# Performance work log

Hardware: AMD Instinct MI355X
Metric: run time of the kernel (lower is better)

The kernel has to match this reference:

```python
import jax, jax.numpy as jnp
import numpy as np

N = 4096          # num_nodes
E = 131072        # num_edges (avg degree 32)
H = 32            # hidden_channels
C_IN, C_OUT = 3, 3
DEPTH = 4
KS = [2000, 1000, 500, 250]  # ceil(ratio * n) per level, ratios = [2000/N, .5, .5, .5]


def gcn(x, A, W, b):
    """GCNConv with improved=True (self-loop fill 2, preserved if already present),
    symmetric normalization, aggregation out[dst] += norm * h[src]."""
    d = jnp.diagonal(A)
    A_hat = A + jnp.diag(jnp.where(d > 0, 0.0, 2.0))
    deg = A_hat.sum(0)                       # in-degree (col sums), as gcn_norm
    dis = jnp.where(deg > 0, jax.lax.rsqrt(deg), 0.0)
    msg = (x @ W) * dis[:, None]
    return (A_hat.T @ msg) * dis[:, None] + b


def augment(A):
    """GraphUNet.augment_adj: add self loops (w=1), square adjacency, drop self loops."""
    n = A.shape[0]
    eye = jnp.eye(n, dtype=A.dtype)
    A_sl = A + eye
    return (A_sl @ A_sl) * (1.0 - eye)


def pool(x, A, p, k):
    """TopKPooling: score = tanh((x.p)/||p||), keep top-k, gate x by score."""
    score = jnp.tanh((x @ p) / jnp.linalg.norm(p))
    vals, perm = jax.lax.top_k(score, k)
    return x[perm] * vals[:, None], A[perm][:, perm], perm


def setup_inputs() -> dict:
    key = jax.random.key(0)
    ks = jax.random.split(key, 12)
    x = jax.random.normal(ks[0], (N, C_IN), jnp.float32)
    edge_index = jax.random.randint(ks[1], (2, E), 0, N, dtype=jnp.int64)
    s = 0.1
    return {
        "x": x,
        "edge_index": edge_index,
        "W0": jax.random.normal(ks[2], (C_IN, H)) * s,
        "b0": jnp.zeros((H,), jnp.float32),
        "Wd": jax.random.normal(ks[3], (DEPTH, H, H)) * s,
        "bd": jnp.zeros((DEPTH, H), jnp.float32),
        "P": jax.random.normal(ks[4], (DEPTH, H)) * s,
        "Wu": jax.random.normal(ks[5], (DEPTH - 1, H, H)) * s,
        "bu": jnp.zeros((DEPTH - 1, H), jnp.float32),
        "Wlast": jax.random.normal(ks[6], (H, C_OUT)) * s,
        "blast": jnp.zeros((C_OUT,), jnp.float32),
    }


def reference(x, edge_index, W0, b0, Wd, bd, P, Wu, bu, Wlast, blast):
    # dense adjacency; duplicate edges accumulate like coalesced sparse weights
    A = jnp.zeros((N, N), jnp.float32).at[edge_index[0], edge_index[1]].add(1.0)
    x = jax.nn.relu(gcn(x, A, W0, b0))
    xs, As, perms = [x], [A], []
    for i in range(DEPTH):
        A = augment(A)
        x, A, perm = pool(x, A, P[i], KS[i])
        x = jax.nn.relu(gcn(x, A, Wd[i], bd[i]))
        if i < DEPTH - 1:
            xs.append(x)
            As.append(A)
        perms.append(perm)
    for i in range(DEPTH):
        j = DEPTH - 1 - i
        res = xs[j]
        up = jnp.zeros_like(res).at[perms[j]].set(x)  # unpool
        x = res + up                                   # sum_res=True
        if i < DEPTH - 1:
            x = jax.nn.relu(gcn(x, As[j], Wu[i], bu[i]))
        else:
            x = gcn(x, As[j], Wlast, blast)
    return jax.nn.log_softmax(x, axis=1)
```

## Files before the change

kernel.cpp:

```cpp
#include <hip/hip_runtime.h>
#include <math.h>

#define H 32
#define N0 4096
#define EMAX 131072
#define APSTR (4096 * 32)

typedef __attribute__((ext_vector_type(4))) float floatx4;
typedef __attribute__((ext_vector_type(8))) short short8;

__device__ __forceinline__ unsigned short f2bf_bits(float v) {
    union { float f; unsigned u; } c;
    c.f = v;
    unsigned lsb = (c.u >> 16) & 1u;
    c.u += 0x7fffu + lsb;
    return (unsigned short)(c.u >> 16);
}

__global__ void fill_sentinel_kernel(float* out, int n) {
    int t = blockIdx.x * 256 + threadIdx.x;
    if (t < n) out[t] = 9.0f;
}

__global__ void build_stats_kernel(const int* __restrict__ ei, int E, int* __restrict__ rowcnt,
                                   int* __restrict__ rowcntD, int* __restrict__ diagcnt) {
    int t = blockIdx.x * 256 + threadIdx.x;
    if (t >= E) return;
    int s = ei[t], d = ei[E + t];
    if ((unsigned)s >= N0 || (unsigned)d >= N0) return;
    atomicAdd(&rowcnt[s], 1);
    atomicAdd(&rowcntD[d], 1);
    if (s == d) atomicAdd(&diagcnt[s], 1);
}

__global__ __launch_bounds__(1024) void scan2_kernel(const int* __restrict__ cntA, int* __restrict__ rowpA,
                                                     int* __restrict__ curA, const int* __restrict__ cntB,
                                                     int* __restrict__ rowpB, int* __restrict__ curB) {
    __shared__ int part[1024];
    int tid = threadIdx.x;
    for (int pass = 0; pass < 2; pass++) {
        const int* cnt = pass ? cntB : cntA;
        int* rowp = pass ? rowpB : rowpA;
        int* cur = pass ? curB : curA;
        int base = tid * 4;
        int local[4];
        int s = 0;
#pragma unroll
        for (int i = 0; i < 4; i++) { local[i] = s; s += cnt[base + i]; }
        part[tid] = s;
        __syncthreads();
        for (int off = 1; off < 1024; off <<= 1) {
            int v = (tid >= off) ? part[tid - off] : 0;
            __syncthreads();
            part[tid] += v;
            __syncthreads();
        }
        int pre = (tid == 0) ? 0 : part[tid - 1];
#pragma unroll
        for (int i = 0; i < 4; i++) { rowp[base + i] = pre + local[i]; cur[base + i] = pre + local[i]; }
        if (tid == 1023) rowp[N0] = pre + s;
        __syncthreads();
    }
}

__global__ void fill_csr_kernel(const int* __restrict__ ei, int E, int* __restrict__ cursor,
                                int* __restrict__ cols, int* __restrict__ cursorD,
                                int* __restrict__ srcs) {
    int t = blockIdx.x * 256 + threadIdx.x;
    if (t >= E) return;
    int s = ei[t], d = ei[E + t];
    if ((unsigned)s >= N0 || (unsigned)d >= N0) return;
    int pos = atomicAdd(&cursor[s], 1);
    cols[pos] = d;
    int posD = atomicAdd(&cursorD[d], 1);
    srcs[posD] = s;
}

__global__ __launch_bounds__(256) void aug0_kernel(const int* __restrict__ rowp, const int* __restrict__ cols,
                                                   const int* __restrict__ perm, const int* __restrict__ invperm,
                                                   int kOut, int ldC, float* __restrict__ C) {
    __shared__ float row[2048];
    int a = blockIdx.x;
    int tid = threadIdx.x;
    for (int j = tid; j < ldC; j += 256) row[j] = 0.f;
    __syncthreads();
    if (a < kOut) {
        int pa = perm[a];
        int s0 = rowp[pa], s1 = rowp[pa + 1];
        for (int e = s0 + tid; e < s1; e += 256) {
            int k = cols[e];
            int ip = invperm[k];
            if (ip >= 0) atomicAdd(&row[ip], 2.0f);
            int t1 = rowp[k + 1];
            for (int e2 = rowp[k]; e2 < t1; ++e2) {
                int ip2 = invperm[cols[e2]];
                if (ip2 >= 0) atomicAdd(&row[ip2], 1.0f);
            }
        }
    }
    __syncthreads();
    for (int j = tid; j < ldC; j += 256) C[(long)a * ldC + j] = (j == a) ? 0.f : row[j];
}

__global__ void gather_rows_kernel(const float* __restrict__ M, int ldM, const int* __restrict__ perm,
                                   int kOut, float* __restrict__ Gr) {
    int k = blockIdx.x * 256 + threadIdx.x;
    int a = blockIdx.y;
    if (k >= ldM) return;
    float v = 0.f;
    if (a < kOut) {
        int pa = perm[a];
        v = M[(long)pa * ldM + k] + (k == pa ? 1.f : 0.f);
    }
    Gr[(long)a * ldM + k] = v;
}

__global__ void gather_rows_bf16_kernel(const float* __restrict__ M, int ldM, const int* __restrict__ perm,
                                        int kOut, unsigned short* __restrict__ Gr) {
    int k = blockIdx.x * 256 + threadIdx.x;
    int a = blockIdx.y;
    if (k >= ldM) return;
    float v = 0.f;
    if (a < kOut) {
        int pa = perm[a];
        v = M[(long)pa * ldM + k] + (k == pa ? 1.f : 0.f);
    }
    Gr[(long)a * ldM + k] = f2bf_bits(v);
}

__global__ void gather_cols_kernel(const float* __restrict__ M, int ldM, const int* __restrict__ perm,
                                   int kOut, float* __restrict__ Gc, int ldC) {
    int b = blockIdx.x * 256 + threadIdx.x;
    int k = blockIdx.y;
    if (b >= ldC) return;
    float v = 0.f;
    if (b < kOut) {
        int pb = perm[b];
        v = M[(long)k * ldM + pb] + (k == pb ? 1.f : 0.f);
    }
    Gc[(long)k * ldC + b] = v;
}

__global__ void gather_colsT_bf16_kernel(const float* __restrict__ M, int ldM,
                                         const int* __restrict__ perm, int kOut,
                                         unsigned short* __restrict__ GcT) {
    __shared__ float t[32][33];
    __shared__ int pb[32];
    int b0 = blockIdx.x * 32, k0 = blockIdx.y * 32;
    int tx = threadIdx.x, ty = threadIdx.y;
    if (ty == 0) pb[tx] = (b0 + tx < kOut) ? perm[b0 + tx] : -1;
    __syncthreads();
    for (int y = ty; y < 32; y += 8) {
        int k = k0 + y;
        int pbx = pb[tx];
        float v = 0.f;
        if (pbx >= 0) v = M[(long)k * ldM + pbx] + (k == pbx ? 1.f : 0.f);
        t[y][tx] = v;
    }
    __syncthreads();
    for (int y = ty; y < 32; y += 8)
        GcT[(long)(b0 + y) * ldM + k0 + tx] = f2bf_bits(t[tx][y]);
}

__global__ __launch_bounds__(256) void mfma_aug_kernel(const unsigned short* __restrict__ Aop,
                                                       const unsigned short* __restrict__ Bop,
                                                       float* __restrict__ C, int K, int ldC, int kchunk) {
    __shared__ __align__(16) unsigned short lA[64 * 32];
    __shared__ __align__(16) unsigned short lB[64 * 32];
    const int tid = threadIdx.x;
    const int lane = tid & 63;
    const int w = tid >> 6;
    const int a0 = blockIdx.y * 64, b0 = blockIdx.x * 64;
    const int kbase = blockIdx.z * kchunk;
    const int r0 = tid >> 2;
    const int c8 = (tid & 3) * 8;
    const unsigned short* gA = Aop + (long)(a0 + r0) * K + kbase + c8;
    const unsigned short* gB = Bop + (long)(b0 + r0) * K + kbase + c8;
    const int wm = (w & 1) * 32;
    const int wn = (w >> 1) * 32;
    const int lm = lane & 15;
    const int quad = lane >> 4;
    floatx4 acc[2][2];
#pragma unroll
    for (int i = 0; i < 2; i++)
#pragma unroll
        for (int j = 0; j < 2; j++) {
            floatx4 z = {0.f, 0.f, 0.f, 0.f};
            acc[i][j] = z;
        }
    for (int k0 = 0; k0 < kchunk; k0 += 32) {
        short8 va = *(const short8*)(gA + k0);
        short8 vb = *(const short8*)(gB + k0);
        __syncthreads();
        *(short8*)&lA[r0 * 32 + c8] = va;
        *(short8*)&lB[r0 * 32 + c8] = vb;
        __syncthreads();
        short8 af[2], bf[2];
#pragma unroll
        for (int mi = 0; mi < 2; mi++) af[mi] = *(const short8*)&lA[(wm + mi * 16 + lm) * 32 + quad * 8];
#pragma unroll
        for (int ni = 0; ni < 2; ni++) bf[ni] = *(const short8*)&lB[(wn + ni * 16 + lm) * 32 + quad * 8];
#pragma unroll
        for (int mi = 0; mi < 2; mi++)
#pragma unroll
            for (int ni = 0; ni < 2; ni++)
                acc[mi][ni] = __builtin_amdgcn_mfma_f32_16x16x32_bf16(af[mi], bf[ni], acc[mi][ni], 0, 0, 0);
    }
#pragma unroll
    for (int mi = 0; mi < 2; mi++)
#pragma unroll
        for (int ni = 0; ni < 2; ni++) {
            int col = b0 + wn + ni * 16 + lm;
#pragma unroll
            for (int r = 0; r < 4; r++) {
                int row = a0 + wm + mi * 16 + quad * 4 + r;
                if (row != col) atomicAdd(&C[(long)row * ldC + col], acc[mi][ni][r]);
            }
        }
}

__global__ __launch_bounds__(256) void gemm64_kernel(const float* __restrict__ Gr,
                                                     const float* __restrict__ Gc,
                                                     float* __restrict__ Cpart, int K, int ldC, int kchunk) {
    __shared__ float As[32][68];
    __shared__ float Bs[32][68];
    const int tid = threadIdx.x;
    const int a0 = blockIdx.y * 64, b0 = blockIdx.x * 64;
    const int kbase = blockIdx.z * kchunk;
    float* Cz = Cpart + (long)blockIdx.z * ldC * ldC;
    const int tx = tid & 15, ty = tid >> 4;
    const int lr = tid >> 2;
    const int lk = (tid & 3) * 8;
    const int bb = tid & 63;
    const int kr = (tid >> 6) * 8;
    const float* gA = Gr + (long)(a0 + lr) * K + lk + kbase;
    const float* gB = Gc + (long)(kr + kbase) * ldC + b0 + bb;
    float acc[4][4];
#pragma unroll
    for (int i = 0; i < 4; i++)
#pragma unroll
        for (int j = 0; j < 4; j++) acc[i][j] = 0.f;
    for (int k0 = 0; k0 < kchunk; k0 += 32) {
        float a8[8], b8[8];
#pragma unroll
        for (int i = 0; i < 8; i++) a8[i] = gA[k0 + i];
#pragma unroll
        for (int i = 0; i < 8; i++) b8[i] = gB[(long)(k0 + i) * ldC];
        __syncthreads();
#pragma unroll
        for (int i = 0; i < 8; i++) As[lk + i][lr] = a8[i];
#pragma unroll
        for (int i = 0; i < 8; i++) Bs[kr + i][bb] = b8[i];
        __syncthreads();
#pragma unroll
        for (int k = 0; k < 32; k++) {
            floatx4 av = *(const floatx4*)&As[k][ty * 4];
            floatx4 bv = *(const floatx4*)&Bs[k][tx * 4];
#pragma unroll
            for (int i = 0; i < 4; i++)
#pragma unroll
                for (int j = 0; j < 4; j++) acc[i][j] += av[i] * bv[j];
        }
    }
#pragma unroll
    for (int i = 0; i < 4; i++)
#pragma unroll
        for (int j = 0; j < 4; j++) {
            int a = a0 + ty * 4 + i, b = b0 + tx * 4 + j;
            Cz[(long)a * ldC + b] = acc[i][j];
        }
}

__global__ void reduce_part_kernel(const float* __restrict__ Cpart, float* __restrict__ C,
                                   int ldC, int ksplit) {
    int t = blockIdx.x * 256 + threadIdx.x;
    long tot = (long)ldC * ldC;
    if (t >= tot) return;
    float s = 0.f;
    for (int z = 0; z < ksplit; z++) s += Cpart[(long)z * tot + t];
    int a = t / ldC, b = t % ldC;
    C[t] = (a == b) ? 0.f : s;
}

__global__ void colsum_part_kernel(const float* __restrict__ A, float* __restrict__ degp, int ld) {
    int i = blockIdx.x * 256 + threadIdx.x;
    int jb = blockIdx.y;
    int j0 = jb * 64;
    float s0 = 0.f, s1 = 0.f, s2 = 0.f, s3 = 0.f, s4 = 0.f, s5 = 0.f, s6 = 0.f, s7 = 0.f;
    const float* p = A + (long)j0 * ld + i;
#pragma unroll
    for (int jq = 0; jq < 64; jq += 8) {
        float v[8];
#pragma unroll
        for (int q = 0; q < 8; q++) v[q] = p[(long)(jq + q) * ld];
        s0 += v[0]; s1 += v[1]; s2 += v[2]; s3 += v[3];
        s4 += v[4]; s5 += v[5]; s6 += v[6]; s7 += v[7];
    }
    float s = ((s0 + s1) + (s2 + s3)) + ((s4 + s5) + (s6 + s7));
    degp[(long)jb * ld + i] = s;
}

__global__ void msgg_kernel(const float* __restrict__ x, const int* __restrict__ perm,
                            const float* __restrict__ vals, const float* __restrict__ xup,
                            const int* __restrict__ invp, const float* __restrict__ Wb,
                            const float* __restrict__ A, int ld, const float* __restrict__ degp,
                            int nparts, float* __restrict__ dis, float* __restrict__ fixb,
                            float* __restrict__ msg, int n) {
    int idx = blockIdx.x * 256 + threadIdx.x;
    if (idx >= n * 32) return;
    int i = idx >> 5, c = idx & 31;
    float di, fx;
    if (degp) {
        float dsum = 0.f;
        for (int z = 0; z < nparts; z++) dsum += degp[(long)z * ld + i];
        float diag = A[(long)i * ld + i];
        fx = diag > 0.f ? 0.f : 2.f;
        float dg = dsum + fx;
        di = dg > 0.f ? 1.f / sqrtf(dg) : 0.f;
        if (c == 0) { dis[i] = di; fixb[i] = fx; }
    } else {
        di = dis[i];
        fx = fixb[i];
    }
    int src = perm ? perm[i] : i;
    float vs = vals ? vals[i] : 1.f;
    int ip = invp ? invp[i] : -1;
    float s = 0.f;
#pragma unroll
    for (int q = 0; q < 32; q++) {
        float xv = x[(long)src * 32 + q];
        if (ip >= 0) xv += xup[(long)ip * 32 + q];
        s += xv * Wb[q * 32 + c];
    }
    msg[idx] = s * vs * di;
    (void)fx;
}

__global__ __launch_bounds__(256) void aggT_kernel(const float* __restrict__ A,
                                                   const float* __restrict__ msg,
                                                   float* __restrict__ aggp, int n, int ld, int jchunk) {
    __shared__ float As[64][64];
    __shared__ float Ms[64][32];
    const int tid = threadIdx.x;
    const int i0 = blockIdx.x * 64;
    const int il = tid & 63;
    const int cg = tid >> 6;
    const int i = i0 + il;
    const int mrow = tid >> 2;
    const int mc = (tid & 3) * 8;
    float acc[8];
#pragma unroll
    for (int q = 0; q < 8; q++) acc[q] = 0.f;
    const int j0 = blockIdx.y * jchunk;
    for (int jb = j0; jb < j0 + jchunk; jb += 64) {
        float a16[16], m8[8];
#pragma unroll
        for (int q = 0; q < 16; q++) a16[q] = A[(long)(jb + cg + 4 * q) * ld + i0 + il];
#pragma unroll
        for (int q = 0; q < 8; q++) m8[q] = msg[(long)(jb + mrow) * 32 + mc + q];
        __syncthreads();
#pragma unroll
        for (int q = 0; q < 16; q++) As[cg + 4 * q][il] = a16[q];
#pragma unroll
        for (int q = 0; q < 8; q++) Ms[mrow][mc + q] = m8[q];
        __syncthreads();
#pragma unroll
        for (int jl = 0; jl < 64; jl++) {
            float a = As[jl][il];
#pragma unroll
            for (int q = 0; q < 8; q++) acc[q] += a * Ms[jl][cg * 8 + q];
        }
        __syncthreads();
    }
    if (i < n) {
#pragma unroll
        for (int q = 0; q < 8; q++) aggp[(long)blockIdx.y * APSTR + (long)i * 32 + cg * 8 + q] = acc[q];
    }
}

__global__ void epi_sum_kernel(const float* __restrict__ aggp, int jsplit, const float* __restrict__ msg,
                               const float* __restrict__ dis, const float* __restrict__ fixb,
                               const float* __restrict__ bb, float* __restrict__ out, int n, int relu,
                               const float* __restrict__ p, int npow,
                               unsigned long long* __restrict__ keys) {
    __shared__ float psh[32];
    if (p) {
        if (threadIdx.x < 32) psh[threadIdx.x] = p[threadIdx.x];
        __syncthreads();
    }
    int idx = blockIdx.x * 256 + threadIdx.x;
    int tot = (p ? npow : n) * 32;
    if (idx >= tot) return;
    int i = idx >> 5, c = idx & 31;
    float v = 0.f;
    if (i < n) {
        float s = 0.f;
        for (int z = 0; z < jsplit; z++) s += aggp[(long)z * APSTR + idx];
        v = (s + fixb[i] * msg[idx]) * dis[i] + bb[c];
        if (relu) v = fmaxf(v, 0.f);
        out[idx] = v;
    }
    if (p) {
        float pc = psh[c];
        float d = v * pc;
        float nq = pc * pc;
#pragma unroll
        for (int st = 16; st >= 1; st >>= 1) {
            d += __shfl_xor(d, st);
            nq += __shfl_xor(nq, st);
        }
        if (c == 0) {
            unsigned long long kk = 0ULL;
            if (i < n) {
                float sc = tanhf(d / sqrtf(nq));
                unsigned u = __float_as_uint(sc);
                u = (u & 0x80000000u) ? ~u : (u | 0x80000000u);
                kk = ((unsigned long long)u << 32) | (unsigned)(~i);
            }
            keys[i] = kk;
        }
    }
}

__global__ void msg0_kernel(const float* __restrict__ x, const float* __restrict__ Wb,
                            const int* __restrict__ rowcntD, const int* __restrict__ diagcnt,
                            float* __restrict__ dis, float* __restrict__ fixb,
                            float* __restrict__ msg, int n) {
    int idx = blockIdx.x * 256 + threadIdx.x;
    if (idx >= n * 32) return;
    int i = idx >> 5, c = idx & 31;
    float fx = diagcnt[i] > 0 ? 0.f : 2.f;
    float dg = (float)rowcntD[i] + fx;
    float di = dg > 0.f ? 1.f / sqrtf(dg) : 0.f;
    if (c == 0) { dis[i] = di; fixb[i] = fx; }
    float s = x[i * 3] * Wb[c] + x[i * 3 + 1] * Wb[32 + c] + x[i * 3 + 2] * Wb[64 + c];
    msg[idx] = s * di;
}

__global__ void msg3up_kernel(const float* __restrict__ res, const float* __restrict__ xup,
                              const int* __restrict__ invp, const float* __restrict__ Wb,
                              const float* __restrict__ dis, float* __restrict__ msg, int n) {
    int idx = blockIdx.x * 256 + threadIdx.x;
    if (idx >= n * 3) return;
    int i = idx / 3, c = idx % 3;
    int ip = invp[i];
    float s = 0.f;
#pragma unroll
    for (int q = 0; q < 32; q++) {
        float xv = res[(long)i * 32 + q];
        if (ip >= 0) xv += xup[(long)ip * 32 + q];
        s += xv * Wb[q * 3 + c];
    }
    msg[idx] = s * dis[i];
}

__global__ void cscagg_epi_keys_kernel(const int* __restrict__ rowpD, const int* __restrict__ srcs,
                                       const float* __restrict__ msg, const float* __restrict__ dis,
                                       const float* __restrict__ fixb, const float* __restrict__ bb,
                                       float* __restrict__ out, int n, const float* __restrict__ p,
                                       unsigned long long* __restrict__ keys) {
    __shared__ float psh[32];
    if (threadIdx.x < 32) psh[threadIdx.x] = p[threadIdx.x];
    __syncthreads();
    int idx = blockIdx.x * 256 + threadIdx.x;
    if (idx >= n * 32) return;
    int i = idx >> 5, c = idx & 31;
    float acc = 0.f;
    int e0 = rowpD[i], e1 = rowpD[i + 1];
    for (int e = e0; e < e1; e++) acc += msg[(long)srcs[e] * 32 + c];
    float v = (acc + fixb[i] * msg[idx]) * dis[i] + bb[c];
    v = fmaxf(v, 0.f);
    out[idx] = v;
    float pc = psh[c];
    float d = v * pc;
    float nq = pc * pc;
#pragma unroll
    for (int st = 16; st >= 1; st >>= 1) {
        d += __shfl_xor(d, st);
        nq += __shfl_xor(nq, st);
    }
    if (c == 0) {
        float sc = tanhf(d / sqrtf(nq));
        unsigned u = __float_as_uint(sc);
        u = (u & 0x80000000u) ? ~u : (u | 0x80000000u);
        keys[i] = ((unsigned long long)u << 32) | (unsigned)(~i);
    }
}

__global__ void cscagg_lsm_kernel(const int* __restrict__ rowpD, const int* __restrict__ srcs,
                                  const float* __restrict__ msg, const float* __restrict__ dis,
                                  const float* __restrict__ fixb, const float* __restrict__ bb,
                                  float* __restrict__ out, int n) {
    int i = blockIdx.x * 256 + threadIdx.x;
    if (i >= n) return;
    float a0 = 0.f, a1 = 0.f, a2 = 0.f;
    int e0 = rowpD[i], e1 = rowpD[i + 1];
    for (int e = e0; e < e1; e++) {
        const float* m = &msg[(long)srcs[e] * 3];
        a0 += m[0]; a1 += m[1]; a2 += m[2];
    }
    float di = dis[i], fx = fixb[i];
    float v0 = (a0 + fx * msg[i * 3]) * di + bb[0];
    float v1 = (a1 + fx * msg[i * 3 + 1]) * di + bb[1];
    float v2 = (a2 + fx * msg[i * 3 + 2]) * di + bb[2];
    float m = fmaxf(v0, fmaxf(v1, v2));
    float s = expf(v0 - m) + expf(v1 - m) + expf(v2 - m);
    float l = m + logf(s);
    out[i * 3] = v0 - l;
    out[i * 3 + 1] = v1 - l;
    out[i * 3 + 2] = v2 - l;
}

__global__ __launch_bounds__(256) void topk_rank_kernel(const unsigned long long* __restrict__ keys,
                                                        int npow, int k, int* __restrict__ perm,
                                                        float* __restrict__ vals,
                                                        int* __restrict__ invperm) {
    __shared__ unsigned long long ks[4096];
    __shared__ int psum[256];
    const int tid = threadIdx.x;
    for (int t = tid; t < npow; t += 256) ks[t] = keys[t];
    __syncthreads();
    const int m = tid & 15;
    const int chunk = tid >> 4;
    const int myi = blockIdx.x * 16 + m;
    unsigned long long my = ks[myi];
    const int cl = npow >> 4;
    const unsigned long long* base = &ks[chunk * cl];
    int r = 0;
#pragma unroll 4
    for (int j = 0; j < cl; j++) r += (base[j] > my) ? 1 : 0;
    psum[chunk * 16 + m] = r;
    __syncthreads();
    if (tid < 16) {
        int mk_i = blockIdx.x * 16 + tid;
        unsigned long long mk = ks[mk_i];
        int rank = 0;
#pragma unroll
        for (int c = 0; c < 16; c++) rank += psum[c * 16 + tid];
        invperm[mk_i] = (rank < k) ? rank : -1;
        if (rank < k) {
            perm[rank] = (int)(~(unsigned)mk);
            unsigned u = (unsigned)(mk >> 32);
            u = (u & 0x80000000u) ? (u ^ 0x80000000u) : ~u;
            vals[rank] = __uint_as_float(u);
        }
    }
}

static void run_gcn_dense(hipStream_t st, const float* A, int n, int ld, const float* x,
                          const int* perm, const float* vals, const float* xup, const int* invp,
                          const float* Wt, const float* bt, int relu, float* out, float* degp,
                          float* aggp, float* dis, float* fixb, float* msgb, int computeDeg,
                          const float* pnext, int npow_next, unsigned long long* keys) {
    if (computeDeg) {
        dim3 gcs(ld / 256 > 0 ? ld / 256 : 1, ld / 64);
        colsum_part_kernel<<<gcs, 256, 0, st>>>(A, degp, ld);
    }
    int gm = (n * H + 255) / 256;
    msgg_kernel<<<gm, 256, 0, st>>>(x, perm, vals, xup, invp, Wt, A, ld,
                                    computeDeg ? degp : nullptr, ld / 64, dis, fixb, msgb, n);
    int jsplit = ld / 256 > 0 ? ld / 256 : 1;
    int ajc = ld / jsplit;
    dim3 ga(ld / 64, jsplit);
    aggT_kernel<<<ga, 256, 0, st>>>(A, msgb, aggp, n, ld, ajc);
    int gme = ((pnext ? npow_next : n) * H + 255) / 256;
    epi_sum_kernel<<<gme, 256, 0, st>>>(aggp, jsplit, msgb, dis, fixb, bt, out, n, relu,
                                        pnext, npow_next, keys);
}

extern "C" void kernel_launch(void* const* d_in, const int* in_sizes, int n_in,
                              void* d_out, int out_size, void* d_ws, size_t ws_size,
                              hipStream_t stream) {
    const float* x0f = (const float*)d_in[0];
    const int* eidx = (const int*)d_in[1];
    const float* W0f = (const float*)d_in[2];
    const float* b0f = (const float*)d_in[3];
    const float* Wdf = (const float*)d_in[4];
    const float* bdf = (const float*)d_in[5];
    const float* Pf = (const float*)d_in[6];
    const float* Wuf = (const float*)d_in[7];
    const float* buf2 = (const float*)d_in[8];
    const float* Wlf = (const float*)d_in[9];
    const float* blf = (const float*)d_in[10];
    const int E = in_sizes[1] / 2;

    unsigned char* w = (unsigned char*)d_ws;
    size_t off = 0;
    auto alloc = [&](size_t bytes) -> void* {
        void* p = w + off;
        off += (bytes + 255) & ~(size_t)255;
        return p;
    };
    int* rowcnt = (int*)alloc(N0 * 4);
    int* rowcntD = (int*)alloc(N0 * 4);
    int* diagcnt = (int*)alloc(N0 * 4);
    int* rowp = (int*)alloc((N0 + 1) * 4);
    int* rowpD = (int*)alloc((N0 + 1) * 4);
    int* cursor = (int*)alloc(N0 * 4);
    int* cursorD = (int*)alloc(N0 * 4);
    int* cols = (int*)alloc((size_t)EMAX * 4);
    int* srcs = (int*)alloc((size_t)EMAX * 4);
    float* dis0 = (float*)alloc(N0 * 4);
    float* fixb0 = (float*)alloc(N0 * 4);
    unsigned long long* keys = (unsigned long long*)alloc((size_t)N0 * 8);
    float* A1 = (float*)alloc((size_t)2048 * 2048 * 4);
    float* A2 = (float*)alloc((size_t)1024 * 1024 * 4);
    float* A3 = (float*)alloc((size_t)512 * 512 * 4);
    float* A4 = (float*)alloc((size_t)256 * 256 * 4);
    float* Gr = (float*)alloc((size_t)1024 * 2048 * 4);
    float* Gc = (float*)alloc((size_t)2048 * 1024 * 4);
    unsigned short* Grb = (unsigned short*)alloc((size_t)1024 * 2048 * 2);
    unsigned short* GcTb = (unsigned short*)alloc((size_t)1024 * 2048 * 2);
    float* Cpart = (float*)alloc((size_t)8 * 512 * 512 * 4);
    float* degp = (float*)alloc((size_t)32 * 2048 * 4);
    float* aggp = (float*)alloc((size_t)8 * APSTR * 4);
    float* xs0 = (float*)alloc((size_t)N0 * H * 4);
    float* xs1 = (float*)alloc((size_t)2000 * H * 4);
    float* xs2 = (float*)alloc((size_t)1000 * H * 4);
    float* xs3 = (float*)alloc((size_t)500 * H * 4);
    float* xtB = (float*)alloc((size_t)N0 * H * 4);
    float* xtC = (float*)alloc((size_t)N0 * H * 4);
    float* msgb = (float*)alloc((size_t)N0 * H * 4);
    float* disL = (float*)alloc((size_t)4 * N0 * 4);
    float* fixbL = (float*)alloc((size_t)4 * N0 * 4);
    int* invpermL = (int*)alloc((size_t)4 * N0 * 4);
    const int ksz[4] = {2000, 1000, 500, 250};
    int* perm[4];
    float* vals[4];
    for (int i = 0; i < 4; i++) perm[i] = (int*)alloc((size_t)ksz[i] * 4);
    for (int i = 0; i < 4; i++) vals[i] = (float*)alloc((size_t)ksz[i] * 4);

    if (off > ws_size) {
        fill_sentinel_kernel<<<(out_size + 255) / 256, 256, 0, stream>>>((float*)d_out, out_size);
        return;
    }

    const int nlvl[5] = {N0, 2000, 1000, 500, 250};
    const int ldl[5] = {N0, 2048, 1024, 512, 256};
    const int npw[4] = {4096, 2048, 1024, 512};
    float* Afp[5] = {nullptr, A1, A2, A3, A4};
    float* xsb[4] = {xs0, xs1, xs2, xs3};

    hipMemsetAsync(rowcnt, 0, (size_t)N0 * 3 * 4, stream);
    build_stats_kernel<<<(E + 255) / 256, 256, 0, stream>>>(eidx, E, rowcnt, rowcntD, diagcnt);
    scan2_kernel<<<1, 1024, 0, stream>>>(rowcnt, rowp, cursor, rowcntD, rowpD, cursorD);
    fill_csr_kernel<<<(E + 255) / 256, 256, 0, stream>>>(eidx, E, cursor, cols, cursorD, srcs);

    msg0_kernel<<<(N0 * H + 255) / 256, 256, 0, stream>>>(x0f, W0f, rowcntD, diagcnt, dis0, fixb0,
                                                          msgb, N0);
    cscagg_epi_keys_kernel<<<(N0 * H + 255) / 256, 256, 0, stream>>>(rowpD, srcs, msgb, dis0, fixb0,
                                                                     b0f, xs0, N0, Pf, keys);
    float* xcur = xs0;

    for (int i = 0; i < 4; ++i) {
        int kk = ksz[i], ldn = ldl[i + 1];
        topk_rank_kernel<<<npw[i] / 16, 256, 0, stream>>>(keys, npw[i], kk, perm[i], vals[i],
                                                          invpermL + i * N0);
        if (i == 0) {
            aug0_kernel<<<ldn, 256, 0, stream>>>(rowp, cols, perm[0], invpermL, kk, ldn, A1);
        } else if (i == 1) {
            int ldM = ldl[i];
            dim3 gr((ldM + 255) / 256, ldn);
            gather_rows_bf16_kernel<<<gr, 256, 0, stream>>>(Afp[i], ldM, perm[i], kk, Grb);
            dim3 gt(ldn / 32, ldM / 32);
            gather_colsT_bf16_kernel<<<gt, dim3(32, 8), 0, stream>>>(Afp[i], ldM, perm[i], kk, GcTb);
            hipMemsetAsync(Afp[i + 1], 0, (size_t)ldn * ldn * 4, stream);
            int ksplit = 4;
            int kchunk = ldM / ksplit;
            dim3 gg(ldn / 64, ldn / 64, ksplit);
            mfma_aug_kernel<<<gg, 256, 0, stream>>>(Grb, GcTb, Afp[i + 1], ldM, ldn, kchunk);
        } else {
            int ldM = ldl[i];
            dim3 gr((ldM + 255) / 256, ldn);
            gather_rows_kernel<<<gr, 256, 0, stream>>>(Afp[i], ldM, perm[i], kk, Gr);
            dim3 gc((ldn + 255) / 256, ldM);
            gather_cols_kernel<<<gc, 256, 0, stream>>>(Afp[i], ldM, perm[i], kk, Gc, ldn);
            int ksplit = 8;
            int kchunk = ldM / ksplit;
            dim3 gg(ldn / 64, ldn / 64, ksplit);
            gemm64_kernel<<<gg, 256, 0, stream>>>(Gr, Gc, Cpart, ldM, ldn, kchunk);
            long tot = (long)ldn * ldn;
            reduce_part_kernel<<<(tot + 255) / 256, 256, 0, stream>>>(Cpart, Afp[i + 1], ldn, ksplit);
        }
        float* outx = (i < 3) ? xsb[i + 1] : xtB;
        const float* pnext = (i < 3) ? (Pf + (i + 1) * H) : nullptr;
        int npow_next = (i < 3) ? npw[i + 1] : 0;
        run_gcn_dense(stream, Afp[i + 1], kk, ldn, xcur, perm[i], vals[i], nullptr, nullptr,
                      Wdf + i * (H * H), bdf + i * H, 1, outx, degp, aggp, disL + i * N0,
                      fixbL + i * N0, msgb, 1, pnext, npow_next, keys);
        xcur = outx;
    }

    for (int i = 0; i < 4; ++i) {
        int j = 3 - i;
        int nj = nlvl[j];
        if (i < 3) {
            float* outx = (xcur == xtB) ? xtC : xtB;
            run_gcn_dense(stream, Afp[j], nj, ldl[j], xsb[j], nullptr, nullptr, xcur,
                          invpermL + j * N0, Wuf + i * (H * H), buf2 + i * H, 1, outx, degp, aggp,
                          disL + (j - 1) * N0, fixbL + (j - 1) * N0, msgb, 0, nullptr, 0, nullptr);
            xcur = outx;
        } else {
            msg3up_kernel<<<(N0 * 3 + 255) / 256, 256, 0, stream>>>(xs0, xcur, invpermL, Wlf, dis0,
                                                                    msgb, N0);
            cscagg_lsm_kernel<<<(N0 + 255) / 256, 256, 0, stream>>>(rowpD, srcs, msgb, dis0, fixb0,
                                                                    blf, (float*)d_out, N0);
        }
    }
}
```

Baseline: 443.0 us.

## Fuse per-level GCN stages into one persistent kernel with grid barriers

```diff
diff --git a/kernel.cpp b/kernel.cpp
--- a/kernel.cpp
+++ b/kernel.cpp
@@ -15,6 +15,24 @@
     unsigned lsb = (c.u >> 16) & 1u;
     c.u += 0x7fffu + lsb;
     return (unsigned short)(c.u >> 16);
+}
+
+__device__ __forceinline__ void grid_bar(int* bar) {
+    __threadfence();
+    __syncthreads();
+    if (threadIdx.x == 0) {
+        int g = __hip_atomic_load(&bar[1], __ATOMIC_RELAXED, __HIP_MEMORY_SCOPE_AGENT);
+        int t = __hip_atomic_fetch_add(&bar[0], 1, __ATOMIC_ACQ_REL, __HIP_MEMORY_SCOPE_AGENT);
+        if (t == (int)gridDim.x - 1) {
+            __hip_atomic_store(&bar[0], 0, __ATOMIC_RELAXED, __HIP_MEMORY_SCOPE_AGENT);
+            __hip_atomic_store(&bar[1], g + 1, __ATOMIC_RELEASE, __HIP_MEMORY_SCOPE_AGENT);
+        } else {
+            while (__hip_atomic_load(&bar[1], __ATOMIC_ACQUIRE, __HIP_MEMORY_SCOPE_AGENT) == g)
+                __builtin_amdgcn_s_sleep(1);
+        }
+    }
+    __syncthreads();
+    __threadfence();
 }
 
 __global__ void fill_sentinel_kernel(float* out, int n) {
@@ -63,17 +81,34 @@
     }
 }
 
-__global__ void fill_csr_kernel(const int* __restrict__ ei, int E, int* __restrict__ cursor,
-                                int* __restrict__ cols, int* __restrict__ cursorD,
-                                int* __restrict__ srcs) {
-    int t = blockIdx.x * 256 + threadIdx.x;
-    if (t >= E) return;
-    int s = ei[t], d = ei[E + t];
-    if ((unsigned)s >= N0 || (unsigned)d >= N0) return;
-    int pos = atomicAdd(&cursor[s], 1);
-    cols[pos] = d;
-    int posD = atomicAdd(&cursorD[d], 1);
-    srcs[posD] = s;
+__global__ void fillcsr_msg0_kernel(const int* __restrict__ ei, int E, int* __restrict__ cursor,
+                                    int* __restrict__ cols, int* __restrict__ cursorD,
+                                    int* __restrict__ srcs, const float* __restrict__ x,
+                                    const float* __restrict__ Wb, const int* __restrict__ rcntD,
+                                    const int* __restrict__ diagcnt, float* __restrict__ dis,
+                                    float* __restrict__ fixb, float* __restrict__ msg, int n) {
+    int nf = (E + 255) >> 8;
+    int tid = threadIdx.x;
+    if ((int)blockIdx.x < nf) {
+        int t = blockIdx.x * 256 + tid;
+        if (t >= E) return;
+        int s = ei[t], d = ei[E + t];
+        if ((unsigned)s >= N0 || (unsigned)d >= N0) return;
+        int pos = atomicAdd(&cursor[s], 1);
+        cols[pos] = d;
+        int posD = atomicAdd(&cursorD[d], 1);
+        srcs[posD] = s;
+    } else {
+        int idx = ((int)blockIdx.x - nf) * 256 + tid;
+        if (idx >= n * 32) return;
+        int i = idx >> 5, c = idx & 31;
+        float fx = diagcnt[i] > 0 ? 0.f : 2.f;
+        float dg = (float)rcntD[i] + fx;
+        float di = dg > 0.f ? 1.f / sqrtf(dg) : 0.f;
+        if (c == 0) { dis[i] = di; fixb[i] = fx; }
+        float s = x[i * 3] * Wb[c] + x[i * 3 + 1] * Wb[32 + c] + x[i * 3 + 2] * Wb[64 + c];
+        msg[idx] = s * di;
+    }
 }
 
 __global__ __launch_bounds__(256) void aug0_kernel(const int* __restrict__ rowp, const int* __restrict__ cols,
@@ -102,64 +137,72 @@
     for (int j = tid; j < ldC; j += 256) C[(long)a * ldC + j] = (j == a) ? 0.f : row[j];
 }
 
-__global__ void gather_rows_kernel(const float* __restrict__ M, int ldM, const int* __restrict__ perm,
-                                   int kOut, float* __restrict__ Gr) {
-    int k = blockIdx.x * 256 + threadIdx.x;
-    int a = blockIdx.y;
-    if (k >= ldM) return;
-    float v = 0.f;
-    if (a < kOut) {
-        int pa = perm[a];
-        v = M[(long)pa * ldM + k] + (k == pa ? 1.f : 0.f);
-    }
-    Gr[(long)a * ldM + k] = v;
-}
-
-__global__ void gather_rows_bf16_kernel(const float* __restrict__ M, int ldM, const int* __restrict__ perm,
-                                        int kOut, unsigned short* __restrict__ Gr) {
-    int k = blockIdx.x * 256 + threadIdx.x;
-    int a = blockIdx.y;
-    if (k >= ldM) return;
-    float v = 0.f;
-    if (a < kOut) {
-        int pa = perm[a];
-        v = M[(long)pa * ldM + k] + (k == pa ? 1.f : 0.f);
-    }
-    Gr[(long)a * ldM + k] = f2bf_bits(v);
-}
-
-__global__ void gather_cols_kernel(const float* __restrict__ M, int ldM, const int* __restrict__ perm,
-                                   int kOut, float* __restrict__ Gc, int ldC) {
-    int b = blockIdx.x * 256 + threadIdx.x;
-    int k = blockIdx.y;
-    if (b >= ldC) return;
-    float v = 0.f;
-    if (b < kOut) {
-        int pb = perm[b];
-        v = M[(long)k * ldM + pb] + (k == pb ? 1.f : 0.f);
-    }
-    Gc[(long)k * ldC + b] = v;
-}
-
-__global__ void gather_colsT_bf16_kernel(const float* __restrict__ M, int ldM,
-                                         const int* __restrict__ perm, int kOut,
-                                         unsigned short* __restrict__ GcT) {
+__global__ void gatherAB_bf16_kernel(const float* __restrict__ M, int ldM, const int* __restrict__ perm,
+                                     int kOut, unsigned short* __restrict__ Gr,
+                                     unsigned short* __restrict__ GcT, int ldn) {
     __shared__ float t[32][33];
     __shared__ int pb[32];
-    int b0 = blockIdx.x * 32, k0 = blockIdx.y * 32;
-    int tx = threadIdx.x, ty = threadIdx.y;
-    if (ty == 0) pb[tx] = (b0 + tx < kOut) ? perm[b0 + tx] : -1;
-    __syncthreads();
-    for (int y = ty; y < 32; y += 8) {
-        int k = k0 + y;
-        int pbx = pb[tx];
+    int half = (ldM >> 8) * ldn;
+    int u = blockIdx.x;
+    int tid = threadIdx.x;
+    if (u < half) {
+        int gx = ldM >> 8;
+        int a = u / gx;
+        int k = (u % gx) * 256 + tid;
         float v = 0.f;
-        if (pbx >= 0) v = M[(long)k * ldM + pbx] + (k == pbx ? 1.f : 0.f);
-        t[y][tx] = v;
-    }
-    __syncthreads();
-    for (int y = ty; y < 32; y += 8)
-        GcT[(long)(b0 + y) * ldM + k0 + tx] = f2bf_bits(t[tx][y]);
+        if (a < kOut) {
+            int pa = perm[a];
+            v = M[(long)pa * ldM + k] + (k == pa ? 1.f : 0.f);
+        }
+        Gr[(long)a * ldM + k] = f2bf_bits(v);
+    } else {
+        u -= half;
+        int nbx = ldn >> 5;
+        int bx = u % nbx, by = u / nbx;
+        int b0 = bx * 32, k0 = by * 32;
+        int tx = tid & 31, ty = tid >> 5;
+        if (ty == 0) pb[tx] = (b0 + tx < kOut) ? perm[b0 + tx] : -1;
+        __syncthreads();
+        for (int y = ty; y < 32; y += 8) {
+            int k = k0 + y;
+            int pbx = pb[tx];
+            float v = 0.f;
+            if (pbx >= 0) v = M[(long)k * ldM + pbx] + (k == pbx ? 1.f : 0.f);
+            t[y][tx] = v;
+        }
+        __syncthreads();
+        for (int y = ty; y < 32; y += 8)
+            GcT[(long)(b0 + y) * ldM + k0 + tx] = f2bf_bits(t[tx][y]);
+    }
+}
+
+__global__ void gather_both_kernel(const float* __restrict__ M, int ldM, const int* __restrict__ perm,
+                                   int kOut, float* __restrict__ Gr, float* __restrict__ Gc, int ldn) {
+    int half = (ldM >> 8) * ldn;
+    int u = blockIdx.x;
+    int tid = threadIdx.x;
+    if (u < half) {
+        int gx = ldM >> 8;
+        int a = u / gx;
+        int k = (u % gx) * 256 + tid;
+        float v = 0.f;
+        if (a < kOut) {
+            int pa = perm[a];
+            v = M[(long)pa * ldM + k] + (k == pa ? 1.f : 0.f);
+        }
+        Gr[(long)a * ldM + k] = v;
+    } else {
+        u -= half;
+        int gx = ldn >> 8;
+        int k = u / gx;
+        int b = (u % gx) * 256 + tid;
+        float v = 0.f;
+        if (b < kOut) {
+            int pb2 = perm[b];
+            v = M[(long)k * ldM + pb2] + (k == pb2 ? 1.f : 0.f);
+        }
+        Gc[(long)k * ldn + b] = v;
+    }
 }
 
 __global__ __launch_bounds__(256) void mfma_aug_kernel(const unsigned short* __restrict__ Aop,
@@ -282,176 +325,200 @@
     C[t] = (a == b) ? 0.f : s;
 }
 
-__global__ void colsum_part_kernel(const float* __restrict__ A, float* __restrict__ degp, int ld) {
-    int i = blockIdx.x * 256 + threadIdx.x;
-    int jb = blockIdx.y;
-    int j0 = jb * 64;
-    float s0 = 0.f, s1 = 0.f, s2 = 0.f, s3 = 0.f, s4 = 0.f, s5 = 0.f, s6 = 0.f, s7 = 0.f;
-    const float* p = A + (long)j0 * ld + i;
-#pragma unroll
-    for (int jq = 0; jq < 64; jq += 8) {
-        float v[8];
-#pragma unroll
-        for (int q = 0; q < 8; q++) v[q] = p[(long)(jq + q) * ld];
-        s0 += v[0]; s1 += v[1]; s2 += v[2]; s3 += v[3];
-        s4 += v[4]; s5 += v[5]; s6 += v[6]; s7 += v[7];
-    }
-    float s = ((s0 + s1) + (s2 + s3)) + ((s4 + s5) + (s6 + s7));
-    degp[(long)jb * ld + i] = s;
-}
-
-__global__ void msgg_kernel(const float* __restrict__ x, const int* __restrict__ perm,
-                            const float* __restrict__ vals, const float* __restrict__ xup,
-                            const int* __restrict__ invp, const float* __restrict__ Wb,
-                            const float* __restrict__ A, int ld, const float* __restrict__ degp,
-                            int nparts, float* __restrict__ dis, float* __restrict__ fixb,
-                            float* __restrict__ msg, int n) {
-    int idx = blockIdx.x * 256 + threadIdx.x;
-    if (idx >= n * 32) return;
-    int i = idx >> 5, c = idx & 31;
-    float di, fx;
-    if (degp) {
-        float dsum = 0.f;
-        for (int z = 0; z < nparts; z++) dsum += degp[(long)z * ld + i];
-        float diag = A[(long)i * ld + i];
-        fx = diag > 0.f ? 0.f : 2.f;
-        float dg = dsum + fx;
-        di = dg > 0.f ? 1.f / sqrtf(dg) : 0.f;
-        if (c == 0) { dis[i] = di; fixb[i] = fx; }
-    } else {
-        di = dis[i];
-        fx = fixb[i];
-    }
-    int src = perm ? perm[i] : i;
-    float vs = vals ? vals[i] : 1.f;
-    int ip = invp ? invp[i] : -1;
-    float s = 0.f;
-#pragma unroll
-    for (int q = 0; q < 32; q++) {
-        float xv = x[(long)src * 32 + q];
-        if (ip >= 0) xv += xup[(long)ip * 32 + q];
-        s += xv * Wb[q * 32 + c];
-    }
-    msg[idx] = s * vs * di;
-    (void)fx;
-}
-
-__global__ __launch_bounds__(256) void aggT_kernel(const float* __restrict__ A,
-                                                   const float* __restrict__ msg,
-                                                   float* __restrict__ aggp, int n, int ld, int jchunk) {
+__global__ __launch_bounds__(256) void gcn_coop_kernel(
+    const float* __restrict__ A, int n, int ld, const float* __restrict__ x,
+    const int* __restrict__ perm, const float* __restrict__ vals,
+    const float* __restrict__ xup, const int* __restrict__ invp,
+    const float* __restrict__ Wb, const float* __restrict__ bb, int relu,
+    float* __restrict__ out, float* __restrict__ degp, float* __restrict__ aggp,
+    float* __restrict__ dis, float* __restrict__ fixb, float* __restrict__ msgb,
+    int computeDeg, const float* __restrict__ pnext, int npow,
+    unsigned long long* __restrict__ keys, int knext, int* __restrict__ permn,
+    float* __restrict__ valsn, int* __restrict__ invpermn, int* bar) {
     __shared__ float As[64][64];
     __shared__ float Ms[64][32];
+    __shared__ unsigned long long ks[2048];
+    __shared__ int psum[256];
+    __shared__ float psh[32];
     const int tid = threadIdx.x;
-    const int i0 = blockIdx.x * 64;
-    const int il = tid & 63;
-    const int cg = tid >> 6;
-    const int i = i0 + il;
-    const int mrow = tid >> 2;
-    const int mc = (tid & 3) * 8;
-    float acc[8];
-#pragma unroll
-    for (int q = 0; q < 8; q++) acc[q] = 0.f;
-    const int j0 = blockIdx.y * jchunk;
-    for (int jb = j0; jb < j0 + jchunk; jb += 64) {
-        float a16[16], m8[8];
-#pragma unroll
-        for (int q = 0; q < 16; q++) a16[q] = A[(long)(jb + cg + 4 * q) * ld + i0 + il];
-#pragma unroll
-        for (int q = 0; q < 8; q++) m8[q] = msg[(long)(jb + mrow) * 32 + mc + q];
-        __syncthreads();
-#pragma unroll
-        for (int q = 0; q < 16; q++) As[cg + 4 * q][il] = a16[q];
-#pragma unroll
-        for (int q = 0; q < 8; q++) Ms[mrow][mc + q] = m8[q];
-        __syncthreads();
-#pragma unroll
-        for (int jl = 0; jl < 64; jl++) {
-            float a = As[jl][il];
-#pragma unroll
-            for (int q = 0; q < 8; q++) acc[q] += a * Ms[jl][cg * 8 + q];
-        }
-        __syncthreads();
-    }
-    if (i < n) {
-#pragma unroll
-        for (int q = 0; q < 8; q++) aggp[(long)blockIdx.y * APSTR + (long)i * 32 + cg * 8 + q] = acc[q];
-    }
-}
-
-__global__ void epi_sum_kernel(const float* __restrict__ aggp, int jsplit, const float* __restrict__ msg,
-                               const float* __restrict__ dis, const float* __restrict__ fixb,
-                               const float* __restrict__ bb, float* __restrict__ out, int n, int relu,
-                               const float* __restrict__ p, int npow,
-                               unsigned long long* __restrict__ keys) {
-    __shared__ float psh[32];
-    if (p) {
-        if (threadIdx.x < 32) psh[threadIdx.x] = p[threadIdx.x];
-        __syncthreads();
-    }
-    int idx = blockIdx.x * 256 + threadIdx.x;
-    int tot = (p ? npow : n) * 32;
-    if (idx >= tot) return;
-    int i = idx >> 5, c = idx & 31;
-    float v = 0.f;
-    if (i < n) {
-        float s = 0.f;
-        for (int z = 0; z < jsplit; z++) s += aggp[(long)z * APSTR + idx];
-        v = (s + fixb[i] * msg[idx]) * dis[i] + bb[c];
-        if (relu) v = fmaxf(v, 0.f);
-        out[idx] = v;
-    }
-    if (p) {
-        float pc = psh[c];
-        float d = v * pc;
-        float nq = pc * pc;
-#pragma unroll
-        for (int st = 16; st >= 1; st >>= 1) {
-            d += __shfl_xor(d, st);
-            nq += __shfl_xor(nq, st);
-        }
-        if (c == 0) {
-            unsigned long long kk = 0ULL;
+    const int nb = gridDim.x;
+    const int jsplit0 = (ld >= 256) ? (ld >> 8) : 1;
+    const int jsplit = jsplit0 < 1 ? 1 : jsplit0;
+
+    if (computeDeg) {
+        int gx = ld >> 8;
+        int nunits = gx * (ld >> 6);
+        for (int u = blockIdx.x; u < nunits; u += nb) {
+            int bi = u % gx, jb = u / gx;
+            int i = bi * 256 + tid;
+            int j0 = jb * 64;
+            const float* p = A + (long)j0 * ld + i;
+            float s0 = 0.f, s1 = 0.f, s2 = 0.f, s3 = 0.f, s4 = 0.f, s5 = 0.f, s6 = 0.f, s7 = 0.f;
+#pragma unroll
+            for (int jq = 0; jq < 64; jq += 8) {
+                float v[8];
+#pragma unroll
+                for (int q = 0; q < 8; q++) v[q] = p[(long)(jq + q) * ld];
+                s0 += v[0]; s1 += v[1]; s2 += v[2]; s3 += v[3];
+                s4 += v[4]; s5 += v[5]; s6 += v[6]; s7 += v[7];
+            }
+            float s = ((s0 + s1) + (s2 + s3)) + ((s4 + s5) + (s6 + s7));
+            degp[(long)jb * ld + i] = s;
+        }
+        grid_bar(bar);
+    }
+
+    {
+        int nparts = ld >> 6;
+        int tot = n * 32;
+        for (int idx = blockIdx.x * 256 + tid; idx < tot; idx += nb * 256) {
+            int i = idx >> 5, c = idx & 31;
+            float di, fx;
+            if (computeDeg) {
+                float dsum = 0.f;
+                for (int z = 0; z < nparts; z++) dsum += degp[(long)z * ld + i];
+                float diag = A[(long)i * ld + i];
+                fx = diag > 0.f ? 0.f : 2.f;
+                float dg = dsum + fx;
+                di = dg > 0.f ? 1.f / sqrtf(dg) : 0.f;
+                if (c == 0) { dis[i] = di; fixb[i] = fx; }
+            } else {
+                di = dis[i];
+                fx = fixb[i];
+            }
+            int src = perm ? perm[i] : i;
+            float vs = vals ? vals[i] : 1.f;
+            int ip = invp ? invp[i] : -1;
+            float s = 0.f;
+#pragma unroll
+            for (int q = 0; q < 32; q++) {
+                float xv = x[(long)src * 32 + q];
+                if (ip >= 0) xv += xup[(long)ip * 32 + q];
+                s += xv * Wb[q * 32 + c];
+            }
+            msgb[idx] = s * vs * di;
+            (void)fx;
+        }
+    }
+    grid_bar(bar);
+
+    {
+        int jchunk = ld / jsplit;
+        int rb = ld >> 6;
+        int nunits = rb * jsplit;
+        const int il = tid & 63;
+        const int cg = tid >> 6;
+        const int mrow = tid >> 2;
+        const int mc = (tid & 3) * 8;
+        for (int u = blockIdx.x; u < nunits; u += nb) {
+            int bx = u % rb, jz = u / rb;
+            int i0 = bx * 64;
+            int i = i0 + il;
+            float acc[8];
+#pragma unroll
+            for (int q = 0; q < 8; q++) acc[q] = 0.f;
+            int j0 = jz * jchunk;
+            for (int jb = j0; jb < j0 + jchunk; jb += 64) {
+                float a16[16], m8[8];
+#pragma unroll
+                for (int q = 0; q < 16; q++) a16[q] = A[(long)(jb + cg + 4 * q) * ld + i0 + il];
+#pragma unroll
+                for (int q = 0; q < 8; q++) m8[q] = msgb[(long)(jb + mrow) * 32 + mc + q];
+                __syncthreads();
+#pragma unroll
+                for (int q = 0; q < 16; q++) As[cg + 4 * q][il] = a16[q];
+#pragma unroll
+                for (int q = 0; q < 8; q++) Ms[mrow][mc + q] = m8[q];
+                __syncthreads();
+#pragma unroll
+                for (int jl = 0; jl < 64; jl++) {
+                    float a = As[jl][il];
+#pragma unroll
+                    for (int q = 0; q < 8; q++) acc[q] += a * Ms[jl][cg * 8 + q];
+                }
+                __syncthreads();
+            }
             if (i < n) {
-                float sc = tanhf(d / sqrtf(nq));
-                unsigned u = __float_as_uint(sc);
-                u = (u & 0x80000000u) ? ~u : (u | 0x80000000u);
-                kk = ((unsigned long long)u << 32) | (unsigned)(~i);
-            }
-            keys[i] = kk;
-        }
-    }
-}
-
-__global__ void msg0_kernel(const float* __restrict__ x, const float* __restrict__ Wb,
-                            const int* __restrict__ rowcntD, const int* __restrict__ diagcnt,
-                            float* __restrict__ dis, float* __restrict__ fixb,
-                            float* __restrict__ msg, int n) {
-    int idx = blockIdx.x * 256 + threadIdx.x;
-    if (idx >= n * 32) return;
-    int i = idx >> 5, c = idx & 31;
-    float fx = diagcnt[i] > 0 ? 0.f : 2.f;
-    float dg = (float)rowcntD[i] + fx;
-    float di = dg > 0.f ? 1.f / sqrtf(dg) : 0.f;
-    if (c == 0) { dis[i] = di; fixb[i] = fx; }
-    float s = x[i * 3] * Wb[c] + x[i * 3 + 1] * Wb[32 + c] + x[i * 3 + 2] * Wb[64 + c];
-    msg[idx] = s * di;
-}
-
-__global__ void msg3up_kernel(const float* __restrict__ res, const float* __restrict__ xup,
-                              const int* __restrict__ invp, const float* __restrict__ Wb,
-                              const float* __restrict__ dis, float* __restrict__ msg, int n) {
-    int idx = blockIdx.x * 256 + threadIdx.x;
-    if (idx >= n * 3) return;
-    int i = idx / 3, c = idx % 3;
-    int ip = invp[i];
-    float s = 0.f;
-#pragma unroll
-    for (int q = 0; q < 32; q++) {
-        float xv = res[(long)i * 32 + q];
-        if (ip >= 0) xv += xup[(long)ip * 32 + q];
-        s += xv * Wb[q * 3 + c];
-    }
-    msg[idx] = s * dis[i];
+#pragma unroll
+                for (int q = 0; q < 8; q++) aggp[(long)jz * APSTR + (long)i * 32 + cg * 8 + q] = acc[q];
+            }
+        }
+    }
+    grid_bar(bar);
+
+    {
+        if (pnext) {
+            if (tid < 32) psh[tid] = pnext[tid];
+            __syncthreads();
+        }
+        int tot = (pnext ? npow : n) * 32;
+        for (int idx = blockIdx.x * 256 + tid; idx < tot; idx += nb * 256) {
+            int i = idx >> 5, c = idx & 31;
+            float v = 0.f;
+            if (i < n) {
+                float s = 0.f;
+                for (int z = 0; z < jsplit; z++) s += aggp[(long)z * APSTR + idx];
+                v = (s + fixb[i] * msgb[idx]) * dis[i] + bb[c];
+                if (relu) v = fmaxf(v, 0.f);
+                out[idx] = v;
+            }
+            if (pnext) {
+                float pc = psh[c];
+                float d = v * pc;
+                float nq = pc * pc;
+#pragma unroll
+                for (int st = 16; st >= 1; st >>= 1) {
+                    d += __shfl_xor(d, st);
+                    nq += __shfl_xor(nq, st);
+                }
+                if (c == 0) {
+                    unsigned long long kk = 0ULL;
+                    if (i < n) {
+                        float sc = tanhf(d / sqrtf(nq));
+                        unsigned u = __float_as_uint(sc);
+                        u = (u & 0x80000000u) ? ~u : (u | 0x80000000u);
+                        kk = ((unsigned long long)u << 32) | (unsigned)(~i);
+                    }
+                    keys[i] = kk;
+                }
+            }
+        }
+    }
+
+    if (pnext) {
+        grid_bar(bar);
+        int nunits = npow >> 4;
+        int cl = npow >> 4;
+        for (int u = blockIdx.x; u < nunits; u += nb) {
+            for (int t = tid; t < npow; t += 256) ks[t] = keys[t];
+            __syncthreads();
+            const int m = tid & 15;
+            const int chunk = tid >> 4;
+            int myi = u * 16 + m;
+            unsigned long long my = ks[myi];
+            const unsigned long long* base = &ks[chunk * cl];
+            int r = 0;
+#pragma unroll 4
+            for (int j = 0; j < cl; j++) r += (base[j] > my) ? 1 : 0;
+            psum[chunk * 16 + m] = r;
+            __syncthreads();
+            if (tid < 16) {
+                int mi = u * 16 + tid;
+                unsigned long long mk = ks[mi];
+                int rank = 0;
+#pragma unroll
+                for (int c = 0; c < 16; c++) rank += psum[c * 16 + tid];
+                invpermn[mi] = (rank < knext) ? rank : -1;
+                if (rank < knext) {
+                    permn[rank] = (int)(~(unsigned)mk);
+                    unsigned uu = (unsigned)(mk >> 32);
+                    uu = (uu & 0x80000000u) ? (uu ^ 0x80000000u) : ~uu;
+                    valsn[rank] = __uint_as_float(uu);
+                }
+            }
+            __syncthreads();
+        }
+    }
 }
 
 __global__ void cscagg_epi_keys_kernel(const int* __restrict__ rowpD, const int* __restrict__ srcs,
@@ -485,6 +552,23 @@
         u = (u & 0x80000000u) ? ~u : (u | 0x80000000u);
         keys[i] = ((unsigned long long)u << 32) | (unsigned)(~i);
     }
+}
+
+__global__ void msg3up_kernel(const float* __restrict__ res, const float* __restrict__ xup,
+                              const int* __restrict__ invp, const float* __restrict__ Wb,
+                              const float* __restrict__ dis, float* __restrict__ msg, int n) {
+    int idx = blockIdx.x * 256 + threadIdx.x;
+    if (idx >= n * 3) return;
+    int i = idx / 3, c = idx % 3;
+    int ip = invp[i];
+    float s = 0.f;
+#pragma unroll
+    for (int q = 0; q < 32; q++) {
+        float xv = res[(long)i * 32 + q];
+        if (ip >= 0) xv += xup[(long)ip * 32 + q];
+        s += xv * Wb[q * 3 + c];
+    }
+    msg[idx] = s * dis[i];
 }
 
 __global__ void cscagg_lsm_kernel(const int* __restrict__ rowpD, const int* __restrict__ srcs,
@@ -547,27 +631,6 @@
     }
 }
 
-static void run_gcn_dense(hipStream_t st, const float* A, int n, int ld, const float* x,
-                          const int* perm, const float* vals, const float* xup, const int* invp,
-                          const float* Wt, const float* bt, int relu, float* out, float* degp,
-                          float* aggp, float* dis, float* fixb, float* msgb, int computeDeg,
-                          const float* pnext, int npow_next, unsigned long long* keys) {
-    if (computeDeg) {
-        dim3 gcs(ld / 256 > 0 ? ld / 256 : 1, ld / 64);
-        colsum_part_kernel<<<gcs, 256, 0, st>>>(A, degp, ld);
-    }
-    int gm = (n * H + 255) / 256;
-    msgg_kernel<<<gm, 256, 0, st>>>(x, perm, vals, xup, invp, Wt, A, ld,
-                                    computeDeg ? degp : nullptr, ld / 64, dis, fixb, msgb, n);
-    int jsplit = ld / 256 > 0 ? ld / 256 : 1;
-    int ajc = ld / jsplit;
-    dim3 ga(ld / 64, jsplit);
-    aggT_kernel<<<ga, 256, 0, st>>>(A, msgb, aggp, n, ld, ajc);
-    int gme = ((pnext ? npow_next : n) * H + 255) / 256;
-    epi_sum_kernel<<<gme, 256, 0, st>>>(aggp, jsplit, msgb, dis, fixb, bt, out, n, relu,
-                                        pnext, npow_next, keys);
-}
-
 extern "C" void kernel_launch(void* const* d_in, const int* in_sizes, int n_in,
                               void* d_out, int out_size, void* d_ws, size_t ws_size,
                               hipStream_t stream) {
@@ -594,6 +657,7 @@
     int* rowcnt = (int*)alloc(N0 * 4);
     int* rowcntD = (int*)alloc(N0 * 4);
     int* diagcnt = (int*)alloc(N0 * 4);
+    int* bar = (int*)alloc(256);
     int* rowp = (int*)alloc((N0 + 1) * 4);
     int* rowpD = (int*)alloc((N0 + 1) * 4);
     int* cursor = (int*)alloc(N0 * 4);
@@ -641,29 +705,31 @@
     float* Afp[5] = {nullptr, A1, A2, A3, A4};
     float* xsb[4] = {xs0, xs1, xs2, xs3};
 
-    hipMemsetAsync(rowcnt, 0, (size_t)N0 * 3 * 4, stream);
+    hipMemsetAsync(rowcnt, 0, (size_t)(N0 * 3 * 4 + 256), stream);
     build_stats_kernel<<<(E + 255) / 256, 256, 0, stream>>>(eidx, E, rowcnt, rowcntD, diagcnt);
     scan2_kernel<<<1, 1024, 0, stream>>>(rowcnt, rowp, cursor, rowcntD, rowpD, cursorD);
-    fill_csr_kernel<<<(E + 255) / 256, 256, 0, stream>>>(eidx, E, cursor, cols, cursorD, srcs);
-
-    msg0_kernel<<<(N0 * H + 255) / 256, 256, 0, stream>>>(x0f, W0f, rowcntD, diagcnt, dis0, fixb0,
-                                                          msgb, N0);
+    {
+        int nf = (E + 255) / 256;
+        int nm = (N0 * H + 255) / 256;
+        fillcsr_msg0_kernel<<<nf + nm, 256, 0, stream>>>(eidx, E, cursor, cols, cursorD, srcs,
+                                                         x0f, W0f, rowcntD, diagcnt, dis0, fixb0,
+                                                         msgb, N0);
+    }
     cscagg_epi_keys_kernel<<<(N0 * H + 255) / 256, 256, 0, stream>>>(rowpD, srcs, msgb, dis0, fixb0,
                                                                      b0f, xs0, N0, Pf, keys);
+    topk_rank_kernel<<<npw[0] / 16, 256, 0, stream>>>(keys, npw[0], ksz[0], perm[0], vals[0],
+                                                      invpermL);
     float* xcur = xs0;
 
     for (int i = 0; i < 4; ++i) {
         int kk = ksz[i], ldn = ldl[i + 1];
-        topk_rank_kernel<<<npw[i] / 16, 256, 0, stream>>>(keys, npw[i], kk, perm[i], vals[i],
-                                                          invpermL + i * N0);
         if (i == 0) {
             aug0_kernel<<<ldn, 256, 0, stream>>>(rowp, cols, perm[0], invpermL, kk, ldn, A1);
         } else if (i == 1) {
             int ldM = ldl[i];
-            dim3 gr((ldM + 255) / 256, ldn);
-            gather_rows_bf16_kernel<<<gr, 256, 0, stream>>>(Afp[i], ldM, perm[i], kk, Grb);
-            dim3 gt(ldn / 32, ldM / 32);
-            gather_colsT_bf16_kernel<<<gt, dim3(32, 8), 0, stream>>>(Afp[i], ldM, perm[i], kk, GcTb);
+            int half = (ldM >> 8) * ldn;
+            int gridB = half + (ldn >> 5) * (ldM >> 5);
+            gatherAB_bf16_kernel<<<gridB, 256, 0, stream>>>(Afp[i], ldM, perm[i], kk, Grb, GcTb, ldn);
             hipMemsetAsync(Afp[i + 1], 0, (size_t)ldn * ldn * 4, stream);
             int ksplit = 4;
             int kchunk = ldM / ksplit;
@@ -671,10 +737,9 @@
             mfma_aug_kernel<<<gg, 256, 0, stream>>>(Grb, GcTb, Afp[i + 1], ldM, ldn, kchunk);
         } else {
             int ldM = ldl[i];
-            dim3 gr((ldM + 255) / 256, ldn);
-            gather_rows_kernel<<<gr, 256, 0, stream>>>(Afp[i], ldM, perm[i], kk, Gr);
-            dim3 gc((ldn + 255) / 256, ldM);
-            gather_cols_kernel<<<gc, 256, 0, stream>>>(Afp[i], ldM, perm[i], kk, Gc, ldn);
+            int half = (ldM >> 8) * ldn;
+            int gridB = half + (ldn >> 8) * ldM;
+            gather_both_kernel<<<gridB, 256, 0, stream>>>(Afp[i], ldM, perm[i], kk, Gr, Gc, ldn);
             int ksplit = 8;
             int kchunk = ldM / ksplit;
             dim3 gg(ldn / 64, ldn / 64, ksplit);
@@ -684,10 +749,14 @@
         }
         float* outx = (i < 3) ? xsb[i + 1] : xtB;
         const float* pnext = (i < 3) ? (Pf + (i + 1) * H) : nullptr;
-        int npow_next = (i < 3) ? npw[i + 1] : 0;
-        run_gcn_dense(stream, Afp[i + 1], kk, ldn, xcur, perm[i], vals[i], nullptr, nullptr,
-                      Wdf + i * (H * H), bdf + i * H, 1, outx, degp, aggp, disL + i * N0,
-                      fixbL + i * N0, msgb, 1, pnext, npow_next, keys);
+        int npown = (i < 3) ? npw[i + 1] : 0;
+        int kn = (i < 3) ? ksz[i + 1] : 0;
+        gcn_coop_kernel<<<256, 256, 0, stream>>>(
+            Afp[i + 1], kk, ldn, xcur, perm[i], vals[i], nullptr, nullptr,
+            Wdf + i * (H * H), bdf + i * H, 1, outx, degp, aggp,
+            disL + i * N0, fixbL + i * N0, msgb, 1, pnext, npown, keys,
+            kn, (i < 3) ? perm[i + 1] : nullptr, (i < 3) ? vals[i + 1] : nullptr,
+            (i < 3) ? (invpermL + (i + 1) * N0) : nullptr, bar);
         xcur = outx;
     }
 
@@ -696,9 +765,11 @@
         int nj = nlvl[j];
         if (i < 3) {
             float* outx = (xcur == xtB) ? xtC : xtB;
-            run_gcn_dense(stream, Afp[j], nj, ldl[j], xsb[j], nullptr, nullptr, xcur,
-                          invpermL + j * N0, Wuf + i * (H * H), buf2 + i * H, 1, outx, degp, aggp,
-                          disL + (j - 1) * N0, fixbL + (j - 1) * N0, msgb, 0, nullptr, 0, nullptr);
+            gcn_coop_kernel<<<256, 256, 0, stream>>>(
+                Afp[j], nj, ldl[j], xsb[j], nullptr, nullptr, xcur, invpermL + j * N0,
+                Wuf + i * (H * H), buf2 + i * H, 1, outx, degp, aggp,
+                disL + (j - 1) * N0, fixbL + (j - 1) * N0, msgb, 0, nullptr, 0, nullptr,
+                0, nullptr, nullptr, nullptr, bar);
             xcur = outx;
         } else {
             msg3up_kernel<<<(N0 * 3 + 255) / 256, 256, 0, stream>>>(xs0, xcur, invpermL, Wlf, dis0,
```

New measurement: 1.628 ms. +267.6%, slower.
